# Performance work log

Measured on AMD Instinct MI355X. Metric: run time of the kernel, lower is better.

The kernel has to match this reference:

```python
import jax, jax.numpy as jnp
import numpy as np

N = 100000   # nodes
E = 1600000  # directed edges (avg degree 16)
D = 128      # num_feature == hidden_channels


def setup_inputs() -> dict:
    key = jax.random.key(0)
    ks = jax.random.split(key, 8)
    s = 1.0 / np.sqrt(D)
    x = jax.random.normal(ks[0], (N, D), jnp.float32)
    edge_index = jax.random.randint(ks[1], (2, E), 0, N, dtype=jnp.int32)
    W1 = jax.random.normal(ks[2], (D, D), jnp.float32) * s
    W2 = jax.random.normal(ks[3], (D, D), jnp.float32) * s
    W3 = jax.random.normal(ks[4], (D, D), jnp.float32) * s
    b1 = jnp.zeros((D,), jnp.float32)
    b2 = jnp.zeros((D,), jnp.float32)
    b3 = jnp.zeros((D,), jnp.float32)
    return {"x": x, "edge_index": edge_index, "W1": W1, "b1": b1,
            "W2": W2, "b2": b2, "W3": W3, "b3": b3}


def reference(x, edge_index, W1, b1, W2, b2, W3, b3):
    # GCNConv with added self-loops and symmetric normalization:
    #   out = D^{-1/2} (A + I) D^{-1/2} (x W) + b
    loops = jnp.arange(N, dtype=edge_index.dtype)
    src = jnp.concatenate([edge_index[0], loops])  # [E+N]
    dst = jnp.concatenate([edge_index[1], loops])
    deg = jax.ops.segment_sum(jnp.ones_like(dst, x.dtype), dst, num_segments=N)
    dinv = jax.lax.rsqrt(deg)                      # deg >= 1 (self-loops)
    norm = dinv[src] * dinv[dst]                   # [E+N]

    def conv(h, W, b):
        h = h @ W                                   # [N, D] dense GEMM
        msg = h[src] * norm[:, None]                # gather + scale [E+N, D]
        return jax.ops.segment_sum(msg, dst, num_segments=N) + b

    # dropout is identity in eval mode
    h = jax.nn.relu(conv(x, W1, b1))
    h = jax.nn.relu(conv(h, W2, b2))
    return conv(h, W3, b3)
```

## Files before the change

### kernel.cpp

```cpp
#include <hip/hip_runtime.h>
#include <hip/hip_fp16.h>

#define DFEAT 128
#define BNODES 256
#define BSHIFT 8
#define B1CHUNK 4096
#define SLABC 8192
#define TPB_TILES 2

typedef _Float16 f16x8 __attribute__((ext_vector_type(8)));
typedef _Float16 f16x4 __attribute__((ext_vector_type(4)));
typedef float f32x4 __attribute__((ext_vector_type(4)));


__global__ __launch_bounds__(256) void bin_k(const int* __restrict__ src, const int* __restrict__ dst,
                                             int* __restrict__ gcnt, unsigned int* __restrict__ slab,
                                             int E, int nbuck) {
    __shared__ int cnt[512];
    __shared__ int off[512];
    __shared__ int gbase[512];
    __shared__ int sd[256];
    __shared__ unsigned int buf[B1CHUNK];
    __shared__ unsigned short bid[B1CHUNK];
    int t = threadIdx.x;
    int base = blockIdx.x * B1CHUNK;
    int nloc = E - base;
    if (nloc > B1CHUNK) nloc = B1CHUNK;
    cnt[t] = 0;
    cnt[t + 256] = 0;
    __syncthreads();
    int k = t;
    for (; k + 768 < nloc; k += 1024) {
        int d0 = dst[base + k], d1 = dst[base + k + 256], d2 = dst[base + k + 512], d3 = dst[base + k + 768];
        atomicAdd(&cnt[d0 >> BSHIFT], 1);
        atomicAdd(&cnt[d1 >> BSHIFT], 1);
        atomicAdd(&cnt[d2 >> BSHIFT], 1);
        atomicAdd(&cnt[d3 >> BSHIFT], 1);
    }
    for (; k < nloc; k += 256) atomicAdd(&cnt[dst[base + k] >> BSHIFT], 1);
    __syncthreads();
    int v0 = cnt[2 * t], v1 = cnt[2 * t + 1];
    int tsum = v0 + v1;
    sd[t] = tsum;
    __syncthreads();
    for (int o = 1; o < 256; o <<= 1) {
        int x = (t >= o) ? sd[t - o] : 0;
        __syncthreads();
        sd[t] += x;
        __syncthreads();
    }
    int texcl = sd[t] - tsum;
    off[2 * t] = texcl;
    off[2 * t + 1] = texcl + v0;
    if (2 * t < nbuck && v0 > 0) gbase[2 * t] = atomicAdd(&gcnt[2 * t], v0);
    if (2 * t + 1 < nbuck && v1 > 0) gbase[2 * t + 1] = atomicAdd(&gcnt[2 * t + 1], v1);
    __syncthreads();
    k = t;
    for (; k + 768 < nloc; k += 1024) {
        int d0 = dst[base + k], d1 = dst[base + k + 256], d2 = dst[base + k + 512], d3 = dst[base + k + 768];
        int s0 = src[base + k], s1 = src[base + k + 256], s2 = src[base + k + 512], s3 = src[base + k + 768];
        int b0 = d0 >> BSHIFT, b1_ = d1 >> BSHIFT, b2_ = d2 >> BSHIFT, b3_ = d3 >> BSHIFT;
        int r0 = atomicAdd(&off[b0], 1); buf[r0] = ((unsigned)s0 << BSHIFT) | (unsigned)(d0 & (BNODES - 1)); bid[r0] = (unsigned short)b0;
        int r1 = atomicAdd(&off[b1_], 1); buf[r1] = ((unsigned)s1 << BSHIFT) | (unsigned)(d1 & (BNODES - 1)); bid[r1] = (unsigned short)b1_;
        int r2 = atomicAdd(&off[b2_], 1); buf[r2] = ((unsigned)s2 << BSHIFT) | (unsigned)(d2 & (BNODES - 1)); bid[r2] = (unsigned short)b2_;
        int r3 = atomicAdd(&off[b3_], 1); buf[r3] = ((unsigned)s3 << BSHIFT) | (unsigned)(d3 & (BNODES - 1)); bid[r3] = (unsigned short)b3_;
    }
    for (; k < nloc; k += 256) {
        int d = dst[base + k];
        int s = src[base + k];
        int b = d >> BSHIFT;
        int r = atomicAdd(&off[b], 1);
        buf[r] = ((unsigned)s << BSHIFT) | (unsigned)(d & (BNODES - 1));
        bid[r] = (unsigned short)b;
    }
    __syncthreads();
    k = t;
    for (; k + 768 < nloc; k += 1024) {
#pragma unroll
        for (int u = 0; u < 4; ++u) {
            int kk = k + u * 256;
            int b = bid[kk];
            int o0 = off[b] - cnt[b];
            int pos = gbase[b] + (kk - o0);
            if (pos < SLABC) slab[(size_t)b * SLABC + pos] = buf[kk];
        }
    }
    for (; k < nloc; k += 256) {
        int b = bid[k];
        int o0 = off[b] - cnt[b];
        int pos = gbase[b] + (k - o0);
        if (pos < SLABC) slab[(size_t)b * SLABC + pos] = buf[k];
    }
}

__global__ __launch_bounds__(256) void bucketAB_k(const unsigned int* __restrict__ slab,
                                                  const int* __restrict__ gcnt,
                                                  int* __restrict__ rp, float* __restrict__ dinv,
                                                  int* __restrict__ cols, int N, int nbuck) {
    __shared__ int cnt[256];
    __shared__ int cur[256];
    __shared__ int psum[256];
    __shared__ int outb[SLABC];
    int t = threadIdx.x;
    int b = blockIdx.x;
    int n0 = b << BSHIFT;
    int nn = N - n0;
    if (nn > BNODES) nn = BNODES;
    int ne_raw = gcnt[b];
    int ne = ne_raw > SLABC ? SLABC : ne_raw;
    const unsigned int* sl = slab + (size_t)b * SLABC;
    int part = 0;
    for (int i = t; i < b; i += 256) part += gcnt[i];
    psum[t] = part;
    cnt[t] = 0;
    __syncthreads();
    for (int o = 128; o > 0; o >>= 1) {
        if (t < o) psum[t] += psum[t + o];
        __syncthreads();
    }
    int base = psum[0];
    int k = t;
    for (; k + 768 < ne; k += 1024) {
        unsigned a0 = sl[k], a1 = sl[k + 256], a2 = sl[k + 512], a3 = sl[k + 768];
        atomicAdd(&cnt[a0 & (BNODES - 1)], 1);
        atomicAdd(&cnt[a1 & (BNODES - 1)], 1);
        atomicAdd(&cnt[a2 & (BNODES - 1)], 1);
        atomicAdd(&cnt[a3 & (BNODES - 1)], 1);
    }
    for (; k < ne; k += 256) atomicAdd(&cnt[sl[k] & (BNODES - 1)], 1);
    __syncthreads();
    int deg = cnt[t];
    for (int o = 1; o < 256; o <<= 1) {
        int x = (t >= o) ? cnt[t - o] : 0;
        __syncthreads();
        cnt[t] += x;
        __syncthreads();
    }
    int excl = cnt[t] - deg;
    if (t < nn) {
        rp[n0 + t] = base + excl;
        dinv[n0 + t] = rsqrtf((float)(deg + 1));
    }
    if (b == nbuck - 1 && t == 0) rp[N] = base + ne_raw;
    cur[t] = excl;
    __syncthreads();
    k = t;
    for (; k + 768 < ne; k += 1024) {
        unsigned a0 = sl[k], a1 = sl[k + 256], a2 = sl[k + 512], a3 = sl[k + 768];
        int p0 = atomicAdd(&cur[a0 & (BNODES - 1)], 1); outb[p0] = (int)(a0 >> BSHIFT);
        int p1 = atomicAdd(&cur[a1 & (BNODES - 1)], 1); outb[p1] = (int)(a1 >> BSHIFT);
        int p2 = atomicAdd(&cur[a2 & (BNODES - 1)], 1); outb[p2] = (int)(a2 >> BSHIFT);
        int p3 = atomicAdd(&cur[a3 & (BNODES - 1)], 1); outb[p3] = (int)(a3 >> BSHIFT);
    }
    for (; k < ne; k += 256) {
        unsigned a = sl[k];
        int p = atomicAdd(&cur[a & (BNODES - 1)], 1);
        outb[p] = (int)(a >> BSHIFT);
    }
    __syncthreads();
    k = t;
    for (; k + 768 < ne; k += 1024) {
        int o0 = outb[k], o1 = outb[k + 256], o2 = outb[k + 512], o3 = outb[k + 768];
        cols[base + k] = o0;
        cols[base + k + 256] = o1;
        cols[base + k + 512] = o2;
        cols[base + k + 768] = o3;
    }
    for (; k < ne; k += 256) cols[base + k] = outb[k];
}

__global__ __launch_bounds__(256) void packW_k(const float* __restrict__ W0, const float* __restrict__ W1,
                                               const float* __restrict__ W2,
                                               const float* __restrict__ b0, const float* __restrict__ b1,
                                               const float* __restrict__ b2,
                                               _Float16* __restrict__ wpk, float* __restrict__ bp,
                                               int* __restrict__ gcnt) {
    int idx = blockIdx.x * 256 + threadIdx.x;
    int layer = idx >> 14;
    int e = idx & 16383;
    int k = e >> 7;
    int nn = e & 127;
    const float* W = (layer == 0) ? W0 : ((layer == 1) ? W1 : W2);
    int ksrc = (layer == 0) ? k : (((k & 7) << 4) | (k >> 3));
    float v = W[ksrc * DFEAT + nn];
    int kc = k >> 5, quad = (k >> 3) & 3, j = k & 7;
    int ct = nn >> 4;
    int pos = ((ct * 4 + kc) * 64 + quad * 16 + (nn & 15)) * 8 + j;
    wpk[(size_t)layer * 16384 + pos] = (_Float16)v;
    if (idx < 384) {
        int l = idx >> 7, p = idx & 127;
        int c = ((p & 7) << 4) | (p >> 3);
        const float* bb = (l == 0) ? b0 : ((l == 1) ? b1 : b2);
        bp[l * 128 + p] = bb[c];
    }
    if (idx < 512) gcnt[idx] = 0;
}


__device__ inline f16x8 ldA8(const float* p) {
    float4 a = *(const float4*)p;
    float4 b = *(const float4*)(p + 4);
    return f16x8{(_Float16)a.x, (_Float16)a.y, (_Float16)a.z, (_Float16)a.w,
                 (_Float16)b.x, (_Float16)b.y, (_Float16)b.z, (_Float16)b.w};
}
__device__ inline f16x8 ldA8(const __half* p) { return *(const f16x8*)p; }
__device__ inline f16x8 zero8() {
    return f16x8{(_Float16)0.f, (_Float16)0.f, (_Float16)0.f, (_Float16)0.f,
                 (_Float16)0.f, (_Float16)0.f, (_Float16)0.f, (_Float16)0.f};
}

template <typename TIN>
__global__ __launch_bounds__(256) void gemmP_k(const TIN* __restrict__ A, const _Float16* __restrict__ wfrag,
                                               const float* __restrict__ dinv, __half* __restrict__ C,
                                               int n, int ntiles) {
    __shared__ _Float16 al[8192];
    __shared__ _Float16 wl[16384];
    const int tid = threadIdx.x;
    const int wv_ = tid >> 6;
    const int lane = tid & 63;
    const int t0 = blockIdx.x * TPB_TILES;
    const int chunk = tid & 15;
    const int rsub = tid >> 4;
    const int kcS = chunk >> 2, quadS = chunk & 3;
    const int swzS = (kcS << 1) ^ (quadS & 1);

    for (int c = tid; c < 2048; c += 256)
        *(f16x8*)&wl[c * 8] = *(const f16x8*)&wfrag[c * 8];

    f16x8 pre[4];
    {
        int row0 = t0 * 64;
#pragma unroll
        for (int p = 0; p < 4; ++p) {
            int gr = row0 + p * 16 + rsub;
            pre[p] = (gr < n) ? ldA8(&A[(size_t)gr * DFEAT + chunk * 8]) : zero8();
        }
    }
    for (int tt = 0; tt < TPB_TILES; ++tt) {
        int tile = t0 + tt;
        if (tile >= ntiles) break;
        int row0 = tile * 64;
#pragma unroll
        for (int p = 0; p < 4; ++p) {
            int idx = (p * 4 + kcS) * 64 + quadS * 16 + rsub;
            *(f16x8*)&al[(idx ^ swzS) * 8] = pre[p];
        }
        __syncthreads();
        if (tt + 1 < TPB_TILES && tile + 1 < ntiles) {
            int nrow0 = (tile + 1) * 64;
#pragma unroll
            for (int p = 0; p < 4; ++p) {
                int gr = nrow0 + p * 16 + rsub;
                pre[p] = (gr < n) ? ldA8(&A[(size_t)gr * DFEAT + chunk * 8]) : zero8();
            }
        }
        f16x8 af[4];
        const int swzR = (lane >> 4) & 1;
#pragma unroll
        for (int kc = 0; kc < 4; ++kc) {
            int idx = (wv_ * 4 + kc) * 64 + lane;
            af[kc] = *(f16x8*)&al[(idx ^ (kc << 1) ^ swzR) * 8];
        }
        const int quad = lane >> 4, cb = lane & 15;
        const int rbase = row0 + wv_ * 16 + quad * 4;
        float ds[4];
#pragma unroll
        for (int r = 0; r < 4; ++r) ds[r] = (rbase + r < n) ? dinv[rbase + r] : 0.f;
        f32x4 acc[8];
#pragma unroll
        for (int ct = 0; ct < 8; ++ct) acc[ct] = (f32x4){0.f, 0.f, 0.f, 0.f};
#pragma unroll
        for (int ct = 0; ct < 8; ++ct) {
#pragma unroll
            for (int kc = 0; kc < 4; ++kc) {
                f16x8 bf = *(f16x8*)&wl[((ct * 4 + kc) * 64 + lane) * 8];
                acc[ct] = __builtin_amdgcn_mfma_f32_16x16x32_f16(af[kc], bf, acc[ct], 0, 0, 0);
            }
        }
#pragma unroll
        for (int r = 0; r < 4; ++r) {
            int gr = rbase + r;
            if (gr < n) {
                f16x8 o;
#pragma unroll
                for (int ct = 0; ct < 8; ++ct) o[ct] = (_Float16)(acc[ct][r] * ds[r]);
                *(f16x8*)&C[(size_t)gr * DFEAT + cb * 8] = o;
            }
        }
        __syncthreads();
    }
}


__device__ inline float2 agg_row(const __half* __restrict__ T, const int* __restrict__ rowptr,
                                 const int* __restrict__ cols, int wid, int lane, int fb) {
    float2 t0 = __half22float2(*(const __half2*)(T + (size_t)wid * DFEAT + fb));
    float ax = t0.x;
    float ay = t0.y;
    int s = rowptr[wid], e = rowptr[wid + 1];
    for (int p = s; p < e; ) {
        int take = e - p;
        if (take > 64) take = 64;
        int q = p + lane;
        if (q >= e) q = e - 1;
        int ci = cols[q];
        int j = 0;
        for (; j + 8 <= take; j += 8) {
            int c0 = __builtin_amdgcn_readlane(ci, j + 0);
            int c1 = __builtin_amdgcn_readlane(ci, j + 1);
            int c2 = __builtin_amdgcn_readlane(ci, j + 2);
            int c3 = __builtin_amdgcn_readlane(ci, j + 3);
            int c4 = __builtin_amdgcn_readlane(ci, j + 4);
            int c5 = __builtin_amdgcn_readlane(ci, j + 5);
            int c6 = __builtin_amdgcn_readlane(ci, j + 6);
            int c7 = __builtin_amdgcn_readlane(ci, j + 7);
            float2 v0 = __half22float2(*(const __half2*)(T + (size_t)c0 * DFEAT + fb));
            float2 v1 = __half22float2(*(const __half2*)(T + (size_t)c1 * DFEAT + fb));
            float2 v2 = __half22float2(*(const __half2*)(T + (size_t)c2 * DFEAT + fb));
            float2 v3 = __half22float2(*(const __half2*)(T + (size_t)c3 * DFEAT + fb));
            float2 v4 = __half22float2(*(const __half2*)(T + (size_t)c4 * DFEAT + fb));
            float2 v5 = __half22float2(*(const __half2*)(T + (size_t)c5 * DFEAT + fb));
            float2 v6 = __half22float2(*(const __half2*)(T + (size_t)c6 * DFEAT + fb));
            float2 v7 = __half22float2(*(const __half2*)(T + (size_t)c7 * DFEAT + fb));
            ax += v0.x; ay += v0.y;
            ax += v1.x; ay += v1.y;
            ax += v2.x; ay += v2.y;
            ax += v3.x; ay += v3.y;
            ax += v4.x; ay += v4.y;
            ax += v5.x; ay += v5.y;
            ax += v6.x; ay += v6.y;
            ax += v7.x; ay += v7.y;
        }
        for (; j < take; ++j) {
            int c = __builtin_amdgcn_readlane(ci, j);
            float2 v = __half22float2(*(const __half2*)(T + (size_t)c * DFEAT + fb));
            ax += v.x; ay += v.y;
        }
        p += take;
    }
    return make_float2(ax, ay);
}

__global__ __launch_bounds__(256) void agg_k(const __half* __restrict__ T, const float* __restrict__ dinv,
                                             const int* __restrict__ rowptr, const int* __restrict__ cols,
                                             const float* __restrict__ biasp,
                                             __half* __restrict__ out, int n) {
    int wid = (int)((blockIdx.x * (size_t)blockDim.x + threadIdx.x) >> 6);
    int lane = threadIdx.x & 63;
    if (wid >= n) return;
    int fb = lane * 2;
    float2 a = agg_row(T, rowptr, cols, wid, lane, fb);
    float dw = dinv[wid];
    float ox = fmaxf(dw * a.x + biasp[fb], 0.f);
    float oy = fmaxf(dw * a.y + biasp[fb + 1], 0.f);
    *(__half2*)(out + (size_t)wid * DFEAT + fb) = __floats2half2_rn(ox, oy);
}

__global__ __launch_bounds__(256) void aggF_k(const __half* __restrict__ T, const float* __restrict__ dinv,
                                              const int* __restrict__ rowptr, const int* __restrict__ cols,
                                              const float* __restrict__ biasp,
                                              float* __restrict__ out, int n) {
    int wid = (int)((blockIdx.x * (size_t)blockDim.x + threadIdx.x) >> 6);
    int lane = threadIdx.x & 63;
    if (wid >= n) return;
    int fb = lane * 2;
    float2 a = agg_row(T, rowptr, cols, wid, lane, fb);
    float dw = dinv[wid];
    float ox = dw * a.x + biasp[fb];
    float oy = dw * a.y + biasp[fb + 1];
    int c0 = ((fb & 7) << 4) | (fb >> 3);
    int c1 = (((fb + 1) & 7) << 4) | ((fb + 1) >> 3);
    out[(size_t)wid * DFEAT + c0] = ox;
    out[(size_t)wid * DFEAT + c1] = oy;
}


extern "C" void kernel_launch(void* const* d_in, const int* in_sizes, int n_in,
                              void* d_out, int out_size, void* d_ws, size_t ws_size,
                              hipStream_t stream) {
    const float* x  = (const float*)d_in[0];
    const int*   ei = (const int*)d_in[1];
    const float* W1 = (const float*)d_in[2];
    const float* b1 = (const float*)d_in[3];
    const float* W2 = (const float*)d_in[4];
    const float* b2 = (const float*)d_in[5];
    const float* W3 = (const float*)d_in[6];
    const float* b3 = (const float*)d_in[7];
    float* out = (float*)d_out;

    const int N = in_sizes[0] / DFEAT;
    const int E = in_sizes[1] / 2;
    const int* srcp = ei;
    const int* dstp = ei + E;

    size_t off = 0;
    auto alloc = [&](size_t bytes) -> void* {
        void* p = (char*)d_ws + off;
        off += (bytes + 255) & ~(size_t)255;
        return p;
    };
    const int nbuck = (N + BNODES - 1) / BNODES;

    int*    gcnt = (int*)alloc(2048);
    int*    rp   = (int*)alloc((size_t)(N + 1) * 4);
    float*  dinv = (float*)alloc((size_t)N * 4);
    _Float16* wpk = (_Float16*)alloc((size_t)3 * 16384 * 2);
    float*  bp   = (float*)alloc(3 * 128 * 4);
    unsigned int* slab = (unsigned int*)alloc((size_t)nbuck * SLABC * 4);
    int*    cols = (int*)alloc((size_t)E * 4);
    __half* bufA = (__half*)alloc((size_t)N * DFEAT * 2);
    __half* bufB = (__half*)alloc((size_t)N * DFEAT * 2);

    packW_k<<<192, 256, 0, stream>>>(W1, W2, W3, b1, b2, b3, wpk, bp, gcnt);
    bin_k<<<(E + B1CHUNK - 1) / B1CHUNK, 256, 0, stream>>>(srcp, dstp, gcnt, slab, E, nbuck);
    bucketAB_k<<<nbuck, 256, 0, stream>>>(slab, gcnt, rp, dinv, cols, N, nbuck);

    int ntiles = (N + 63) / 64;
    int gemmGrid = (ntiles + TPB_TILES - 1) / TPB_TILES;
    int aggGrid  = (int)(((size_t)N * 64 + 255) / 256);

    gemmP_k<float><<<gemmGrid, 256, 0, stream>>>(x, wpk, dinv, bufA, N, ntiles);
    agg_k<<<aggGrid, 256, 0, stream>>>(bufA, dinv, rp, cols, bp, bufB, N);

    gemmP_k<__half><<<gemmGrid, 256, 0, stream>>>(bufB, wpk + 16384, dinv, bufA, N, ntiles);
    agg_k<<<aggGrid, 256, 0, stream>>>(bufA, dinv, rp, cols, bp + 128, bufB, N);

    gemmP_k<__half><<<gemmGrid, 256, 0, stream>>>(bufB, wpk + 32768, dinv, bufA, N, ntiles);
    aggF_k<<<aggGrid, 256, 0, stream>>>(bufA, dinv, rp, cols, bp + 256, out, N);
}
```

Measured before the change: 379.4 us.

## Fuse weight packing into binning kernel and load GEMM A fragments directly

```diff
diff --git a/kernel.cpp b/kernel.cpp
--- a/kernel.cpp
+++ b/kernel.cpp
@@ -6,16 +6,21 @@
 #define BSHIFT 8
 #define B1CHUNK 4096
 #define SLABC 8192
-#define TPB_TILES 2
+#define TPB_TILES 3
 
 typedef _Float16 f16x8 __attribute__((ext_vector_type(8)));
 typedef _Float16 f16x4 __attribute__((ext_vector_type(4)));
 typedef float f32x4 __attribute__((ext_vector_type(4)));
 
 
-__global__ __launch_bounds__(256) void bin_k(const int* __restrict__ src, const int* __restrict__ dst,
-                                             int* __restrict__ gcnt, unsigned int* __restrict__ slab,
-                                             int E, int nbuck) {
+__global__ __launch_bounds__(256) void binpack_k(const int* __restrict__ src, const int* __restrict__ dst,
+                                                 int* __restrict__ gcnt, unsigned int* __restrict__ slab,
+                                                 int E, int nbuck, int nbin,
+                                                 const float* __restrict__ W0, const float* __restrict__ W1,
+                                                 const float* __restrict__ W2,
+                                                 const float* __restrict__ b0, const float* __restrict__ b1,
+                                                 const float* __restrict__ b2,
+                                                 _Float16* __restrict__ wpk, float* __restrict__ bp) {
     __shared__ int cnt[512];
     __shared__ int off[512];
     __shared__ int gbase[512];
@@ -23,6 +28,27 @@
     __shared__ unsigned int buf[B1CHUNK];
     __shared__ unsigned short bid[B1CHUNK];
     int t = threadIdx.x;
+    if (blockIdx.x >= nbin) {
+        int idx = (blockIdx.x - nbin) * 256 + t;
+        int layer = idx >> 14;
+        int e = idx & 16383;
+        int k = e >> 7;
+        int nn = e & 127;
+        const float* W = (layer == 0) ? W0 : ((layer == 1) ? W1 : W2);
+        int ksrc = (layer == 0) ? k : (((k & 7) << 4) | (k >> 3));
+        float v = W[ksrc * DFEAT + nn];
+        int kc = k >> 5, quad = (k >> 3) & 3, j = k & 7;
+        int ct = nn >> 4;
+        int pos = ((ct * 4 + kc) * 64 + quad * 16 + (nn & 15)) * 8 + j;
+        wpk[(size_t)layer * 16384 + pos] = (_Float16)v;
+        if (idx < 384) {
+            int l = idx >> 7, p = idx & 127;
+            int c = ((p & 7) << 4) | (p >> 3);
+            const float* bb = (l == 0) ? b0 : ((l == 1) ? b1 : b2);
+            bp[l * 128 + p] = bb[c];
+        }
+        return;
+    }
     int base = blockIdx.x * B1CHUNK;
     int nloc = E - base;
     if (nloc > B1CHUNK) nloc = B1CHUNK;
@@ -59,8 +85,8 @@
     for (; k + 768 < nloc; k += 1024) {
         int d0 = dst[base + k], d1 = dst[base + k + 256], d2 = dst[base + k + 512], d3 = dst[base + k + 768];
         int s0 = src[base + k], s1 = src[base + k + 256], s2 = src[base + k + 512], s3 = src[base + k + 768];
-        int b0 = d0 >> BSHIFT, b1_ = d1 >> BSHIFT, b2_ = d2 >> BSHIFT, b3_ = d3 >> BSHIFT;
-        int r0 = atomicAdd(&off[b0], 1); buf[r0] = ((unsigned)s0 << BSHIFT) | (unsigned)(d0 & (BNODES - 1)); bid[r0] = (unsigned short)b0;
+        int b0_ = d0 >> BSHIFT, b1_ = d1 >> BSHIFT, b2_ = d2 >> BSHIFT, b3_ = d3 >> BSHIFT;
+        int r0 = atomicAdd(&off[b0_], 1); buf[r0] = ((unsigned)s0 << BSHIFT) | (unsigned)(d0 & (BNODES - 1)); bid[r0] = (unsigned short)b0_;
         int r1 = atomicAdd(&off[b1_], 1); buf[r1] = ((unsigned)s1 << BSHIFT) | (unsigned)(d1 & (BNODES - 1)); bid[r1] = (unsigned short)b1_;
         int r2 = atomicAdd(&off[b2_], 1); buf[r2] = ((unsigned)s2 << BSHIFT) | (unsigned)(d2 & (BNODES - 1)); bid[r2] = (unsigned short)b2_;
         int r3 = atomicAdd(&off[b3_], 1); buf[r3] = ((unsigned)s3 << BSHIFT) | (unsigned)(d3 & (BNODES - 1)); bid[r3] = (unsigned short)b3_;
@@ -169,33 +195,6 @@
     for (; k < ne; k += 256) cols[base + k] = outb[k];
 }
 
-__global__ __launch_bounds__(256) void packW_k(const float* __restrict__ W0, const float* __restrict__ W1,
-                                               const float* __restrict__ W2,
-                                               const float* __restrict__ b0, const float* __restrict__ b1,
-                                               const float* __restrict__ b2,
-                                               _Float16* __restrict__ wpk, float* __restrict__ bp,
-                                               int* __restrict__ gcnt) {
-    int idx = blockIdx.x * 256 + threadIdx.x;
-    int layer = idx >> 14;
-    int e = idx & 16383;
-    int k = e >> 7;
-    int nn = e & 127;
-    const float* W = (layer == 0) ? W0 : ((layer == 1) ? W1 : W2);
-    int ksrc = (layer == 0) ? k : (((k & 7) << 4) | (k >> 3));
-    float v = W[ksrc * DFEAT + nn];
-    int kc = k >> 5, quad = (k >> 3) & 3, j = k & 7;
-    int ct = nn >> 4;
-    int pos = ((ct * 4 + kc) * 64 + quad * 16 + (nn & 15)) * 8 + j;
-    wpk[(size_t)layer * 16384 + pos] = (_Float16)v;
-    if (idx < 384) {
-        int l = idx >> 7, p = idx & 127;
-        int c = ((p & 7) << 4) | (p >> 3);
-        const float* bb = (l == 0) ? b0 : ((l == 1) ? b1 : b2);
-        bp[l * 128 + p] = bb[c];
-    }
-    if (idx < 512) gcnt[idx] = 0;
-}
-
 
 __device__ inline f16x8 ldA8(const float* p) {
     float4 a = *(const float4*)p;
@@ -213,56 +212,32 @@
 __global__ __launch_bounds__(256) void gemmP_k(const TIN* __restrict__ A, const _Float16* __restrict__ wfrag,
                                                const float* __restrict__ dinv, __half* __restrict__ C,
                                                int n, int ntiles) {
-    __shared__ _Float16 al[8192];
     __shared__ _Float16 wl[16384];
     const int tid = threadIdx.x;
     const int wv_ = tid >> 6;
     const int lane = tid & 63;
-    const int t0 = blockIdx.x * TPB_TILES;
-    const int chunk = tid & 15;
-    const int rsub = tid >> 4;
-    const int kcS = chunk >> 2, quadS = chunk & 3;
-    const int swzS = (kcS << 1) ^ (quadS & 1);
-
+    const int m = lane & 15;
+    const int q = lane >> 4;
     for (int c = tid; c < 2048; c += 256)
         *(f16x8*)&wl[c * 8] = *(const f16x8*)&wfrag[c * 8];
-
-    f16x8 pre[4];
-    {
-        int row0 = t0 * 64;
-#pragma unroll
-        for (int p = 0; p < 4; ++p) {
-            int gr = row0 + p * 16 + rsub;
-            pre[p] = (gr < n) ? ldA8(&A[(size_t)gr * DFEAT + chunk * 8]) : zero8();
-        }
-    }
-    for (int tt = 0; tt < TPB_TILES; ++tt) {
-        int tile = t0 + tt;
-        if (tile >= ntiles) break;
+    __syncthreads();
+
+    int t0 = blockIdx.x * TPB_TILES;
+    int tend = t0 + TPB_TILES;
+    if (tend > ntiles) tend = ntiles;
+    for (int tile = t0; tile < tend; ++tile) {
         int row0 = tile * 64;
-#pragma unroll
-        for (int p = 0; p < 4; ++p) {
-            int idx = (p * 4 + kcS) * 64 + quadS * 16 + rsub;
-            *(f16x8*)&al[(idx ^ swzS) * 8] = pre[p];
-        }
-        __syncthreads();
-        if (tt + 1 < TPB_TILES && tile + 1 < ntiles) {
-            int nrow0 = (tile + 1) * 64;
-#pragma unroll
-            for (int p = 0; p < 4; ++p) {
-                int gr = nrow0 + p * 16 + rsub;
-                pre[p] = (gr < n) ? ldA8(&A[(size_t)gr * DFEAT + chunk * 8]) : zero8();
-            }
-        }
+        int ga = row0 + wv_ * 16 + m;
         f16x8 af[4];
-        const int swzR = (lane >> 4) & 1;
-#pragma unroll
-        for (int kc = 0; kc < 4; ++kc) {
-            int idx = (wv_ * 4 + kc) * 64 + lane;
-            af[kc] = *(f16x8*)&al[(idx ^ (kc << 1) ^ swzR) * 8];
-        }
-        const int quad = lane >> 4, cb = lane & 15;
-        const int rbase = row0 + wv_ * 16 + quad * 4;
+        if (ga < n) {
+#pragma unroll
+            for (int kc = 0; kc < 4; ++kc)
+                af[kc] = ldA8(&A[(size_t)ga * DFEAT + kc * 32 + q * 8]);
+        } else {
+#pragma unroll
+            for (int kc = 0; kc < 4; ++kc) af[kc] = zero8();
+        }
+        const int rbase = row0 + wv_ * 16 + q * 4;
         float ds[4];
 #pragma unroll
         for (int r = 0; r < 4; ++r) ds[r] = (rbase + r < n) ? dinv[rbase + r] : 0.f;
@@ -284,10 +259,9 @@
                 f16x8 o;
 #pragma unroll
                 for (int ct = 0; ct < 8; ++ct) o[ct] = (_Float16)(acc[ct][r] * ds[r]);
-                *(f16x8*)&C[(size_t)gr * DFEAT + cb * 8] = o;
+                *(f16x8*)&C[(size_t)gr * DFEAT + m * 8] = o;
             }
         }
-        __syncthreads();
     }
 }
 
@@ -411,8 +385,10 @@
     __half* bufA = (__half*)alloc((size_t)N * DFEAT * 2);
     __half* bufB = (__half*)alloc((size_t)N * DFEAT * 2);
 
-    packW_k<<<192, 256, 0, stream>>>(W1, W2, W3, b1, b2, b3, wpk, bp, gcnt);
-    bin_k<<<(E + B1CHUNK - 1) / B1CHUNK, 256, 0, stream>>>(srcp, dstp, gcnt, slab, E, nbuck);
+    const int nbin = (E + B1CHUNK - 1) / B1CHUNK;
+    hipMemsetAsync(gcnt, 0, 2048, stream);
+    binpack_k<<<nbin + 192, 256, 0, stream>>>(srcp, dstp, gcnt, slab, E, nbuck, nbin,
+                                              W1, W2, W3, b1, b2, b3, wpk, bp);
     bucketAB_k<<<nbuck, 256, 0, stream>>>(slab, gcnt, rp, dinv, cols, N, nbuck);
 
     int ntiles = (N + 63) / 64;
```

New measurement: 388.5 us. 1.02x slower.
